# Kernel optimization log

Measured on AMD Instinct MI355X. Metric: run time of the kernel, lower is better.

## Reference

```python
import jax, jax.numpy as jnp
import numpy as np
from jax.ops import segment_sum, segment_max

H, D, HID, L, B = 4, 32, 128, 2, 64  # heads, head_dim, hidden, layers, graphs
NB, NS, NC, NF = 100000, 20000, 10000, 2000


def setup_inputs() -> dict:
    key = jax.random.key(0)
    ks = iter(jax.random.split(key, 64))
    nrm = lambda shape, s=1.0: jax.random.normal(next(ks), shape, jnp.float32) * s
    ridx = lambda n, hi: jax.random.randint(next(ks), (n,), 0, hi, jnp.int32)
    srt = lambda n, hi: jnp.sort(jax.random.randint(next(ks), (n,), 0, hi, jnp.int32))
    return {
        'x_block': nrm((NB, 8)), 'x_spmt': nrm((NS, 10)),
        'x_crane': nrm((NC, 7)), 'x_facility': nrm((NF, 3)),
        'Wp_b': nrm((8, HID), 0.2), 'bp_b': jnp.zeros((HID,), jnp.float32),
        'Wp_s': nrm((10, HID), 0.2), 'bp_s': jnp.zeros((HID,), jnp.float32),
        'Wp_c': nrm((7, HID), 0.2), 'bp_c': jnp.zeros((HID,), jnp.float32),
        'Wp_f': nrm((3, HID), 0.2), 'bp_f': jnp.zeros((HID,), jnp.float32),
        'gat_W': nrm((L, 8, HID, HID), 0.05),
        'gat_as': nrm((L, 8, H, D), 0.1), 'gat_ad': nrm((L, 8, H, D), 0.1),
        'gat_b': jnp.zeros((L, 8, HID), jnp.float32),
        'ln_s': jnp.ones((L, HID), jnp.float32), 'ln_b': jnp.zeros((L, HID), jnp.float32),
        'e_nt_s': ridx(800000, NB), 'e_nt_d': ridx(800000, NS),
        'e_ct_s': ridx(800000, NS), 'e_ct_d': ridx(800000, NB),
        'e_nl_s': ridx(400000, NB), 'e_nl_d': ridx(400000, NC),
        'e_cl_s': ridx(400000, NC), 'e_cl_d': ridx(400000, NB),
        'e_ba_s': ridx(100000, NB), 'e_ba_d': ridx(100000, NF),
        'e_pr_s': ridx(800000, NB), 'e_pr_d': ridx(800000, NB),
        'e_sa_s': ridx(20000, NS), 'e_sa_d': ridx(20000, NF),
        'e_ca_s': ridx(10000, NC), 'e_ca_d': ridx(10000, NF),
        'b_block': srt(NB, B), 'b_spmt': srt(NS, B),
        'b_crane': srt(NC, B), 'b_facility': srt(NF, B),
    }


def layer_norm(x, s, b):
    mu = x.mean(-1, keepdims=True)
    v = ((x - mu) ** 2).mean(-1, keepdims=True)
    return (x - mu) / jnp.sqrt(v + 1e-5) * s + b


def gat(h_src, h_dst, src, dst, W, a_s, a_d, bias):
    # PyG GATConv (shared lin for src/dst, add_self_loops=False, eval mode)
    n_dst = h_dst.shape[0]
    hs = (h_src @ W).reshape(-1, H, D)                 # [Ns,H,D]
    hd = (h_dst @ W).reshape(-1, H, D)                 # [Nd,H,D]
    al_s = (hs * a_s).sum(-1)                          # [Ns,H]
    al_d = (hd * a_d).sum(-1)                          # [Nd,H]
    e = jax.nn.leaky_relu(al_s[src] + al_d[dst], 0.2)  # [E,H]
    m = segment_max(e, dst, num_segments=n_dst)
    m = jnp.where(jnp.isfinite(m), m, 0.0)             # empty segments
    ex = jnp.exp(e - m[dst])
    den = segment_sum(ex, dst, num_segments=n_dst)
    coef = ex / (den[dst] + 1e-16)                     # scatter-softmax
    msg = hs[src] * coef[..., None]                    # [E,H,D]
    out = segment_sum(msg, dst, num_segments=n_dst)
    return out.reshape(n_dst, H * D) + bias


def pool(x, b):
    s = segment_sum(x, b, num_segments=B)
    c = segment_sum(jnp.ones((x.shape[0],), x.dtype), b, num_segments=B)
    return s / jnp.clip(c, 1.0)[:, None]


def reference(x_block, x_spmt, x_crane, x_facility,
              Wp_b, bp_b, Wp_s, bp_s, Wp_c, bp_c, Wp_f, bp_f,
              gat_W, gat_as, gat_ad, gat_b, ln_s, ln_b,
              e_nt_s, e_nt_d, e_ct_s, e_ct_d, e_nl_s, e_nl_d, e_cl_s, e_cl_d,
              e_ba_s, e_ba_d, e_pr_s, e_pr_d, e_sa_s, e_sa_d, e_ca_s, e_ca_d,
              b_block, b_spmt, b_crane, b_facility):
    xb = x_block @ Wp_b + bp_b
    xs = x_spmt @ Wp_s + bp_s
    xc = x_crane @ Wp_c + bp_c
    xf = x_facility @ Wp_f + bp_f
    rels = [(0, 'b', 's', e_nt_s, e_nt_d), (1, 's', 'b', e_ct_s, e_ct_d),
            (2, 'b', 'c', e_nl_s, e_nl_d), (3, 'c', 'b', e_cl_s, e_cl_d),
            (4, 'b', 'f', e_ba_s, e_ba_d), (5, 'b', 'b', e_pr_s, e_pr_d),
            (6, 's', 'f', e_sa_s, e_sa_d), (7, 'c', 'f', e_ca_s, e_ca_d)]
    for l in range(L):
        x = {'b': xb, 's': xs, 'c': xc, 'f': xf}
        acc = {k: [] for k in x}
        for r, st, dt, src, dst in rels:
            acc[dt].append(gat(x[st], x[dt], src, dst,
                               gat_W[l, r], gat_as[l, r], gat_ad[l, r], gat_b[l, r]))
        new = {k: sum(v) / len(v) for k, v in acc.items()}  # HeteroConv mean
        xb = layer_norm(jax.nn.relu(new['b']) + xb, ln_s[l], ln_b[l])
        xs = layer_norm(jax.nn.relu(new['s']) + xs, ln_s[l], ln_b[l])
        xc = layer_norm(jax.nn.relu(new['c']) + xc, ln_s[l], ln_b[l])
        xf = layer_norm(jax.nn.relu(new['f']) + xf, ln_s[l], ln_b[l])
    return jnp.concatenate([pool(xb, b_block), pool(xs, b_spmt),
                            pool(xc, b_crane), pool(xf, b_facility)], axis=-1)
```

## Files before the change

kernel.cpp:

```cpp
#include <hip/hip_runtime.h>
#include <hip/hip_bf16.h>
#include <cstdint>

#define HID 128
#define NHEAD 4
#define NGRAPH 64
#define PCHUNK 32
#define NBIN 64
#define MAXBINW 2048

typedef __attribute__((ext_vector_type(8))) short bf16x8;
typedef __attribute__((ext_vector_type(4))) short bf16x4s;
typedef __attribute__((ext_vector_type(4))) float f32x4;

__device__ __forceinline__ float bf2f(short u) {
    union { float f; unsigned int i; } c;
    c.i = ((unsigned int)(unsigned short)u) << 16;
    return c.f;
}
__device__ __forceinline__ float lrelu(float a) { return (a > 0.f) ? a : 0.2f * a; }

struct PrePack {
    const int* edst[8]; int E[8]; int h_off[9]; int bsh[8];
    int* binCnt;
    const float* px[4]; const float* pW[4]; const float* pb[4]; float* po[4];
    int pN[4]; int pK[4]; int p_off[5];
    const float* gat_W; __hip_bfloat16* Wsw;
    const float* gat_as; const float* gat_ad; float* vecall;
};

__global__ __launch_bounds__(256) void k_pre(PrePack A) {
    int b = blockIdx.x;
    int tid = threadIdx.x;
    if (b < A.h_off[8]) {
        __shared__ int h64[NBIN];
        if (tid < NBIN) h64[tid] = 0;
        __syncthreads();
#pragma unroll
        for (int r = 0; r < 8; ++r) {
            if (b >= A.h_off[r] && b < A.h_off[r + 1]) {
                int e = (b - A.h_off[r]) * 256 + tid;
                if (e < A.E[r]) atomicAdd(&h64[A.edst[r][e] >> A.bsh[r]], 1);
                __syncthreads();
                if (tid < NBIN && h64[tid] > 0) atomicAdd(&A.binCnt[r * NBIN + tid], h64[tid]);
            }
        }
        return;
    }
    b -= A.h_off[8];
    if (b < A.p_off[4]) {
#pragma unroll
        for (int t = 0; t < 4; ++t) {
            if (b >= A.p_off[t] && b < A.p_off[t + 1]) {
                int idx = (b - A.p_off[t]) * 256 + tid;
                if (idx < A.pN[t] * HID) {
                    int row = idx >> 7, c = idx & 127;
                    int K = A.pK[t];
                    float acc = A.pb[t][c];
                    for (int k = 0; k < K; ++k) acc += A.px[t][row * K + k] * A.pW[t][k * HID + c];
                    A.po[t][idx] = acc;
                }
            }
        }
        return;
    }
    b -= A.p_off[4];
    if (b < 1024) {
        int idx = b * 256 + tid;
        int l = idx >> 17;
        int rem = idx & 131071;
        int k = rem >> 10;
        int gc = rem & 1023;
        int rel, n, gobase, Ncols;
        if (gc < 512) {
            int i = gc >> 7;
            rel = (i == 0) ? 0 : (i == 1) ? 2 : (i == 2) ? 4 : 5;
            n = gc; gobase = 0; Ncols = 512;
        } else if (gc < 768) {
            int c2 = gc - 512;
            rel = (c2 >> 7) ? 6 : 1;
            n = c2; gobase = 65536; Ncols = 256;
        } else {
            int c2 = gc - 768;
            rel = (c2 >> 7) ? 7 : 3;
            n = c2; gobase = 98304; Ncols = 256;
        }
        int nl = n & 127;
        float v = A.gat_W[(((size_t)l * 8 + rel) * 128 + k) * 128 + nl];
        size_t dst = (size_t)l * 131072 + gobase + ((size_t)(k >> 3) * Ncols + n) * 8 + (k & 7);
        A.Wsw[dst] = __float2bfloat16(v);
        return;
    }
    b -= 1024;
    {
        int idx = b * 256 + tid;
        if (idx < 16384) {
            int h = idx & 3, k = (idx >> 2) & 127, p = (idx >> 9) & 15, l = idx >> 13;
            int r = p >> 1, side = p & 1;
            const float* W = A.gat_W + (((size_t)l * 8 + r) * 128 + k) * 128;
            const float* a = (side ? A.gat_ad : A.gat_as) + ((size_t)l * 8 + r) * 128;
            float s = 0.f;
#pragma unroll
            for (int j = 0; j < 32; ++j) s += W[h * 32 + j] * a[h * 32 + j];
            A.vecall[((size_t)l * 16 + p) * 512 + k * 4 + h] = s;
        }
    }
}

struct BinPack {
    const int* esrc[8]; const int* edst[8];
    uint2* staging[8];
    int* adj[8]; int* deg[8]; int* offs[8];
    int* binCnt; int* binBase; int* binCur;
    int E[8]; int Nd[8]; int binshift[8];
};

__global__ void k_binscan2(BinPack B) {
    int r = threadIdx.x;
    if (r >= 8) return;
    int run = 0;
    for (int b = 0; b < NBIN; ++b) {
        int c = B.binCnt[r * NBIN + b];
        B.binBase[r * NBIN + b] = run;
        B.binCur[r * NBIN + b] = run;
        run += c;
    }
}

__global__ __launch_bounds__(256) void k_binp1(BinPack B) {
    int r = blockIdx.y;
    int E = B.E[r];
    int sh = B.binshift[r];
    __shared__ int h[NBIN], base[NBIN], rk[NBIN];
    int tid = threadIdx.x;
    for (int e0 = blockIdx.x * 256; e0 < E; e0 += gridDim.x * 256) {
        if (tid < NBIN) { h[tid] = 0; rk[tid] = 0; }
        __syncthreads();
        int e = e0 + tid;
        int valid = e < E;
        int src = 0, dst = 0, bin = 0;
        if (valid) {
            src = B.esrc[r][e];
            dst = B.edst[r][e];
            bin = dst >> sh;
            atomicAdd(&h[bin], 1);
        }
        __syncthreads();
        if (tid < NBIN && h[tid] > 0) base[tid] = atomicAdd(&B.binCur[r * NBIN + tid], h[tid]);
        __syncthreads();
        if (valid) {
            int pos = base[bin] + atomicAdd(&rk[bin], 1);
            B.staging[r][pos] = make_uint2((unsigned)src, (unsigned)dst);
        }
        __syncthreads();
    }
}

__global__ __launch_bounds__(1024) void k_binhist(BinPack B) {
    int r = blockIdx.y, bin = blockIdx.x;
    int sh = B.binshift[r];
    int width = 1 << sh;
    int d0 = bin << sh;
    int Nd = B.Nd[r];
    int ndst = Nd - d0;
    if (ndst > width) ndst = width;
    if (ndst <= 0) return;
    __shared__ int h[MAXBINW];
    int tid = threadIdx.x;
    for (int i = tid; i < width; i += 1024) h[i] = 0;
    __syncthreads();
    int cnt = B.binCnt[r * NBIN + bin];
    const uint2* st = B.staging[r] + B.binBase[r * NBIN + bin];
    for (int i = tid; i < cnt; i += 1024) atomicAdd(&h[(int)st[i].y - d0], 1);
    __syncthreads();
    for (int i = tid; i < ndst; i += 1024) B.deg[r][d0 + i] = h[i];
}

__global__ __launch_bounds__(1024) void k_binp2(BinPack B) {
    int r = blockIdx.y, bin = blockIdx.x;
    int sh = B.binshift[r];
    int width = 1 << sh;
    int d0 = bin << sh;
    int Nd = B.Nd[r];
    int ndst = Nd - d0;
    if (ndst > width) ndst = width;
    if (ndst <= 0) return;
    __shared__ int curs[MAXBINW];
    int tid = threadIdx.x;
    for (int i = tid; i < ndst; i += 1024) curs[i] = B.offs[r][d0 + i];
    __syncthreads();
    int cnt = B.binCnt[r * NBIN + bin];
    const uint2* st = B.staging[r] + B.binBase[r * NBIN + bin];
    int* adj = B.adj[r];
    for (int i = tid; i < cnt; i += 1024) {
        uint2 ed = st[i];
        int slot = atomicAdd(&curs[(int)ed.y - d0], 1);
        adj[slot] = (int)ed.x;
    }
}

struct ScanPack {
    int* deg[8];
    int* offs[8];
    int Nd[8];
};

__global__ void k_scan_part_all(ScanPack P, int* __restrict__ part_all) {
    int r = blockIdx.y;
    int N = P.Nd[r];
    if (blockIdx.x * 256 >= N) return;
    __shared__ int sh[256];
    int t = threadIdx.x, i = blockIdx.x * 256 + t;
    sh[t] = (i < N) ? P.deg[r][i] : 0;
    __syncthreads();
    for (int o = 128; o; o >>= 1) {
        if (t < o) sh[t] += sh[t + o];
        __syncthreads();
    }
    if (t == 0) part_all[r * 512 + blockIdx.x] = sh[0];
}
__global__ void k_scan_top_all(int* __restrict__ part_all, ScanPack P) {
    int r = blockIdx.x;
    int n = (P.Nd[r] + 255) / 256;
    __shared__ int sh[512];
    int t = threadIdx.x;
    int v = (t < n) ? part_all[r * 512 + t] : 0;
    sh[t] = v;
    __syncthreads();
    for (int o = 1; o < 512; o <<= 1) {
        int tmp = (t >= o) ? sh[t - o] : 0;
        __syncthreads();
        sh[t] += tmp;
        __syncthreads();
    }
    if (t < n) part_all[r * 512 + t] = sh[t] - v;
}
__global__ void k_scan_down_all(ScanPack P, const int* __restrict__ part_all) {
    int r = blockIdx.y;
    int N = P.Nd[r];
    if (blockIdx.x * 256 >= N) return;
    __shared__ int sh[256];
    int t = threadIdx.x, i = blockIdx.x * 256 + t;
    int v = (i < N) ? P.deg[r][i] : 0;
    sh[t] = v;
    __syncthreads();
    for (int o = 1; o < 256; o <<= 1) {
        int tmp = (t >= o) ? sh[t - o] : 0;
        __syncthreads();
        sh[t] += tmp;
        __syncthreads();
    }
    if (i < N) P.offs[r][i] = sh[t] - v + part_all[r * 512 + blockIdx.x];
}

__device__ __forceinline__ void gemm_body(char* smemraw, const float* __restrict__ A,
                                          const __hip_bfloat16* __restrict__ Bsw,
                                          __hip_bfloat16* __restrict__ out,
                                          int M, int Ncols, int bx, int by) {
    __hip_bfloat16 (*Alds)[136] = (__hip_bfloat16 (*)[136])smemraw;
    int m0 = bx * 64, n0 = by * 128;
    int t = threadIdx.x;
    for (int i = t; i < 2048; i += 256) {
        int row = i >> 5, ch = i & 31;
        float4 v = make_float4(0.f, 0.f, 0.f, 0.f);
        if (m0 + row < M) v = *(const float4*)(A + (size_t)(m0 + row) * 128 + ch * 4);
        __hip_bfloat16* dp = &Alds[row][ch * 4];
        dp[0] = __float2bfloat16(v.x);
        dp[1] = __float2bfloat16(v.y);
        dp[2] = __float2bfloat16(v.z);
        dp[3] = __float2bfloat16(v.w);
    }
    __syncthreads();
    int w = t >> 6, l = t & 63;
    int lane16 = l & 15, q = l >> 4;
    f32x4 acc[8];
#pragma unroll
    for (int nn = 0; nn < 8; ++nn) acc[nn] = (f32x4){0.f, 0.f, 0.f, 0.f};
    const __hip_bfloat16* arow = &Alds[w * 16 + lane16][q * 8];
#pragma unroll
    for (int kk = 0; kk < 4; ++kk) {
        bf16x8 a = *(const bf16x8*)(arow + kk * 32);
#pragma unroll
        for (int nn = 0; nn < 8; ++nn) {
            size_t boff = ((size_t)(kk * 4 + q) * Ncols + (n0 + nn * 16 + lane16)) * 8;
            bf16x8 b = *(const bf16x8*)(Bsw + boff);
            acc[nn] = __builtin_amdgcn_mfma_f32_16x16x32_bf16(a, b, acc[nn], 0, 0, 0);
        }
    }
    int orow = m0 + w * 16 + q * 4;
#pragma unroll
    for (int nn = 0; nn < 8; ++nn) {
        int col = n0 + nn * 16 + lane16;
#pragma unroll
        for (int r = 0; r < 4; ++r) {
            int row = orow + r;
            if (row < M) out[(size_t)row * Ncols + col] = __float2bfloat16(acc[nn][r]);
        }
    }
}

__device__ __forceinline__ void logits_body(char* smemraw,
                                            const float* const vec[7], float* const outp[7],
                                            const float* __restrict__ x, int N, int nv, int bloc) {
    float (*vs)[128][4] = (float (*)[128][4])smemraw;
    int t = threadIdx.x;
    for (int i = t; i < nv * 512; i += 256) {
        int v = i >> 9, j = i & 511;
        vs[v][j >> 2][j & 3] = vec[v][j];
    }
    __syncthreads();
    int nl = t >> 2, h = t & 3;
    int node = bloc * 64 + nl;
    if (node >= N) return;
    const float* xr = x + (size_t)node * 128;
    float acc[7];
#pragma unroll
    for (int v = 0; v < 7; ++v) acc[v] = 0.f;
#pragma unroll 4
    for (int k = 0; k < 128; ++k) {
        float xv = xr[k];
#pragma unroll
        for (int v = 0; v < 7; ++v)
            if (v < nv) acc[v] += xv * vs[v][k][h];
    }
#pragma unroll
    for (int v = 0; v < 7; ++v)
        if (v < nv) outp[v][node * 4 + h] = acc[v];
}

struct MidPack {
    const float* gA[3]; const __hip_bfloat16* gB[3]; __hip_bfloat16* gO[3];
    int gM[3]; int gNc[3]; int gMB[3]; int g_off[4];
    const float* lvec[4][7]; float* lout[4][7]; const float* lx[4];
    int lN[4]; int lnv[4]; int l_off[5];
};

__global__ __launch_bounds__(256) void k_mid(MidPack M) {
    __shared__ __align__(16) char smem[17408];
    int b = blockIdx.x;
    if (b < M.g_off[3]) {
#pragma unroll
        for (int g = 0; g < 3; ++g) {
            if (b >= M.g_off[g] && b < M.g_off[g + 1]) {
                int local = b - M.g_off[g];
                int bx = local % M.gMB[g];
                int by = local / M.gMB[g];
                gemm_body(smem, M.gA[g], M.gB[g], M.gO[g], M.gM[g], M.gNc[g], bx, by);
            }
        }
        return;
    }
    b -= M.g_off[3];
#pragma unroll
    for (int t = 0; t < 4; ++t) {
        if (b >= M.l_off[t] && b < M.l_off[t + 1]) {
            logits_body(smem, M.lvec[t], M.lout[t], M.lx[t], M.lN[t], M.lnv[t], b - M.l_off[t]);
        }
    }
}

struct RelArg {
    const __hip_bfloat16* hs;
    int hstride;
    int hoff;
    const float* als;
    const float* ald;
    const int* adj;
    const int* off;
    const int* deg;
    const float* bias;
};

__device__ __forceinline__ void dst_body(const RelArg& r0, const RelArg& r1, const RelArg& r2,
                                         int nrel, float inv_nrel, float* __restrict__ x,
                                         const float* __restrict__ ln_s,
                                         const float* __restrict__ ln_b, int N, int bloc) {
    int wv = threadIdx.x >> 6, lane = threadIdx.x & 63;
    int half = lane >> 5, sl = lane & 31;
    int d = bloc * 8 + wv * 2 + half;
    if (d >= N) return;
    int c0 = sl * 4;
    int h = sl >> 3;
    float4 xv = *(const float4*)&x[(size_t)d * HID + c0];
    float rel0 = 0.f, rel1 = 0.f, rel2 = 0.f, rel3 = 0.f;
    for (int rr = 0; rr < nrel; ++rr) {
        const RelArg& R = (rr == 0) ? r0 : (rr == 1) ? r1 : r2;
        int base = R.off[d];
        int dg = R.deg[d];
        float aldh = R.ald[d * NHEAD + h];
        const __hip_bfloat16* hp = R.hs + R.hoff + c0;
        const int hstr = R.hstride;
        const int* ap = R.adj + base;
        const float* als = R.als;
        float a0 = 0.f, a1 = 0.f, a2 = 0.f, a3 = 0.f, den = 0.f;
        int k = 0;
        for (; k + 4 <= dg; k += 4) {
            int s0 = ap[k], s1 = ap[k + 1], s2 = ap[k + 2], s3 = ap[k + 3];
            float w0 = __expf(lrelu(als[s0 * NHEAD + h] + aldh));
            float w1 = __expf(lrelu(als[s1 * NHEAD + h] + aldh));
            float w2 = __expf(lrelu(als[s2 * NHEAD + h] + aldh));
            float w3 = __expf(lrelu(als[s3 * NHEAD + h] + aldh));
            bf16x4s v0 = *(const bf16x4s*)(hp + (size_t)s0 * hstr);
            bf16x4s v1 = *(const bf16x4s*)(hp + (size_t)s1 * hstr);
            bf16x4s v2 = *(const bf16x4s*)(hp + (size_t)s2 * hstr);
            bf16x4s v3 = *(const bf16x4s*)(hp + (size_t)s3 * hstr);
            a0 += w0 * bf2f(v0[0]) + w1 * bf2f(v1[0]) + w2 * bf2f(v2[0]) + w3 * bf2f(v3[0]);
            a1 += w0 * bf2f(v0[1]) + w1 * bf2f(v1[1]) + w2 * bf2f(v2[1]) + w3 * bf2f(v3[1]);
            a2 += w0 * bf2f(v0[2]) + w1 * bf2f(v1[2]) + w2 * bf2f(v2[2]) + w3 * bf2f(v3[2]);
            a3 += w0 * bf2f(v0[3]) + w1 * bf2f(v1[3]) + w2 * bf2f(v2[3]) + w3 * bf2f(v3[3]);
            den += w0 + w1 + w2 + w3;
        }
        for (; k < dg; ++k) {
            int s = ap[k];
            float w = __expf(lrelu(als[s * NHEAD + h] + aldh));
            bf16x4s v = *(const bf16x4s*)(hp + (size_t)s * hstr);
            a0 += w * bf2f(v[0]);
            a1 += w * bf2f(v[1]);
            a2 += w * bf2f(v[2]);
            a3 += w * bf2f(v[3]);
            den += w;
        }
        float inv = 1.f / (den + 1e-16f);
        rel0 += a0 * inv + R.bias[c0];
        rel1 += a1 * inv + R.bias[c0 + 1];
        rel2 += a2 * inv + R.bias[c0 + 2];
        rel3 += a3 * inv + R.bias[c0 + 3];
    }
    float v0 = rel0 * inv_nrel, v1 = rel1 * inv_nrel;
    float v2 = rel2 * inv_nrel, v3 = rel3 * inv_nrel;
    v0 = (v0 > 0.f) ? v0 : 0.f;
    v1 = (v1 > 0.f) ? v1 : 0.f;
    v2 = (v2 > 0.f) ? v2 : 0.f;
    v3 = (v3 > 0.f) ? v3 : 0.f;
    v0 += xv.x; v1 += xv.y; v2 += xv.z; v3 += xv.w;
    float s = v0 + v1 + v2 + v3;
    float ss = v0 * v0 + v1 * v1 + v2 * v2 + v3 * v3;
#pragma unroll
    for (int o = 16; o; o >>= 1) {
        s += __shfl_xor(s, o);
        ss += __shfl_xor(ss, o);
    }
    float mu = s * (1.f / HID);
    float var = ss * (1.f / HID) - mu * mu;
    float rstd = rsqrtf(var + 1e-5f);
    float o0 = (v0 - mu) * rstd * ln_s[c0] + ln_b[c0];
    float o1 = (v1 - mu) * rstd * ln_s[c0 + 1] + ln_b[c0 + 1];
    float o2 = (v2 - mu) * rstd * ln_s[c0 + 2] + ln_b[c0 + 2];
    float o3 = (v3 - mu) * rstd * ln_s[c0 + 3] + ln_b[c0 + 3];
    *(float4*)&x[(size_t)d * HID + c0] = make_float4(o0, o1, o2, o3);
}

struct TypeArg {
    RelArg r0, r1, r2;
    float* x;
    int N;
    int nrel;
    float inv_nrel;
};

__global__ __launch_bounds__(256) void k_dst_all(TypeArg t0, TypeArg t1, TypeArg t2, TypeArg t3,
                                                 int off1, int off2, int off3,
                                                 const float* __restrict__ ln_s,
                                                 const float* __restrict__ ln_b) {
    int b = blockIdx.x;
    if (b < off1) {
        dst_body(t0.r0, t0.r1, t0.r2, t0.nrel, t0.inv_nrel, t0.x, ln_s, ln_b, t0.N, b);
    } else if (b < off2) {
        dst_body(t1.r0, t1.r1, t1.r2, t1.nrel, t1.inv_nrel, t1.x, ln_s, ln_b, t1.N, b - off1);
    } else if (b < off3) {
        dst_body(t2.r0, t2.r1, t2.r2, t2.nrel, t2.inv_nrel, t2.x, ln_s, ln_b, t2.N, b - off2);
    } else {
        dst_body(t3.r0, t3.r1, t3.r2, t3.nrel, t3.inv_nrel, t3.x, ln_s, ln_b, t3.N, b - off3);
    }
}

__global__ void k_pool_all(const float* __restrict__ x0, const float* __restrict__ x1,
                           const float* __restrict__ x2, const float* __restrict__ x3,
                           const int* __restrict__ b0, const int* __restrict__ b1,
                           const int* __restrict__ b2, const int* __restrict__ b3,
                           int N0, int N1, int N2, int N3, float* __restrict__ out) {
    int ty = blockIdx.y;
    const float* x;
    const int* b;
    int N, toff;
    if (ty == 0)      { x = x0; b = b0; N = N0; toff = 0; }
    else if (ty == 1) { x = x1; b = b1; N = N1; toff = 128; }
    else if (ty == 2) { x = x2; b = b2; N = N2; toff = 256; }
    else              { x = x3; b = b3; N = N3; toff = 384; }
    int r0 = blockIdx.x * PCHUNK;
    if (r0 >= N) return;
    int rend = min(r0 + PCHUNK, N);
    int c = threadIdx.x;
    int cur = b[r0];
    float acc = 0.f;
    for (int i = r0; i < rend; ++i) {
        int g = b[i];
        if (g != cur) {
            atomicAdd(&out[cur * 512 + toff + c], acc);
            acc = 0.f;
            cur = g;
        }
        acc += x[(size_t)i * HID + c];
    }
    atomicAdd(&out[cur * 512 + toff + c], acc);
}
__global__ void k_cnt(const int* __restrict__ b0, const int* __restrict__ b1,
                      const int* __restrict__ b2, const int* __restrict__ b3,
                      int N0, int N1, int N2, int N3, float* __restrict__ cnt) {
    int i = blockIdx.x * blockDim.x + threadIdx.x;
    if (i >= 256) return;
    int t = i >> 6, g = i & 63;
    const int* b = (t == 0) ? b0 : (t == 1) ? b1 : (t == 2) ? b2 : b3;
    int N = (t == 0) ? N0 : (t == 1) ? N1 : (t == 2) ? N2 : N3;
    int lo = 0, hi = N;
    while (lo < hi) { int m = (lo + hi) >> 1; if (b[m] < g) lo = m + 1; else hi = m; }
    int s = lo;
    hi = N;
    while (lo < hi) { int m = (lo + hi) >> 1; if (b[m] < g + 1) lo = m + 1; else hi = m; }
    cnt[i] = (float)(lo - s);
}
__global__ void k_div(float* __restrict__ out, const float* __restrict__ cnt) {
    int idx = blockIdx.x * blockDim.x + threadIdx.x;
    if (idx >= NGRAPH * 512) return;
    int g = idx >> 9, c = idx & 511, t = c >> 7;
    out[idx] = out[idx] / fmaxf(cnt[t * NGRAPH + g], 1.0f);
}

extern "C" void kernel_launch(void* const* d_in, const int* in_sizes, int n_in,
                              void* d_out, int out_size, void* d_ws, size_t ws_size,
                              hipStream_t stream) {
    const float* x_in[4] = {(const float*)d_in[0], (const float*)d_in[1],
                            (const float*)d_in[2], (const float*)d_in[3]};
    const float* Wp[4] = {(const float*)d_in[4], (const float*)d_in[6],
                          (const float*)d_in[8], (const float*)d_in[10]};
    const float* bp[4] = {(const float*)d_in[5], (const float*)d_in[7],
                          (const float*)d_in[9], (const float*)d_in[11]};
    const float* gat_W  = (const float*)d_in[12];
    const float* gat_as = (const float*)d_in[13];
    const float* gat_ad = (const float*)d_in[14];
    const float* gat_b  = (const float*)d_in[15];
    const float* ln_s   = (const float*)d_in[16];
    const float* ln_b   = (const float*)d_in[17];
    const int* esrc[8] = {(const int*)d_in[18], (const int*)d_in[20], (const int*)d_in[22],
                          (const int*)d_in[24], (const int*)d_in[26], (const int*)d_in[28],
                          (const int*)d_in[30], (const int*)d_in[32]};
    const int* edst[8] = {(const int*)d_in[19], (const int*)d_in[21], (const int*)d_in[23],
                          (const int*)d_in[25], (const int*)d_in[27], (const int*)d_in[29],
                          (const int*)d_in[31], (const int*)d_in[33]};
    const int* bidx[4] = {(const int*)d_in[34], (const int*)d_in[35],
                          (const int*)d_in[36], (const int*)d_in[37]};
    int E[8];
    {
        const int eidx[8] = {18, 20, 22, 24, 26, 28, 30, 32};
        for (int r = 0; r < 8; ++r) E[r] = in_sizes[eidx[r]];
    }
    const int Kin[4] = {8, 10, 7, 3};
    int N[4];
    for (int t = 0; t < 4; ++t) N[t] = in_sizes[t] / Kin[t];
    const int rel_st[8] = {0, 1, 0, 2, 0, 0, 1, 2};
    const int rel_dt[8] = {1, 0, 2, 0, 3, 0, 3, 3};
    const int rel_hoff[8] = {0, 0, 128, 0, 256, 384, 128, 128};
    const int grp_stride[4] = {512, 256, 256, 0};
    (void)ws_size; (void)n_in;

    char* wbase = (char*)d_ws;
    size_t cur = 0;
    auto alloc = [&](size_t bytes) -> void* {
        void* p = wbase + cur;
        cur += (bytes + 15) & ~(size_t)15;
        return p;
    };
    float* x[4];
    for (int t = 0; t < 4; ++t) x[t] = (float*)alloc((size_t)N[t] * HID * 4);
    __hip_bfloat16* hs_g[3];
    hs_g[0] = (__hip_bfloat16*)alloc((size_t)N[0] * 512 * 2);
    hs_g[1] = (__hip_bfloat16*)alloc((size_t)N[1] * 256 * 2);
    hs_g[2] = (__hip_bfloat16*)alloc((size_t)N[2] * 256 * 2);
    __hip_bfloat16* Wsw = (__hip_bfloat16*)alloc((size_t)2 * 131072 * 2);
    float* vecall = (float*)alloc((size_t)2 * 16 * 512 * 4);
    float *als_[8], *ald_[8];
    int *deg[8], *offs[8], *adj[8];
    uint2* staging[8];
    for (int r = 0; r < 8; ++r) {
        int Ns = N[rel_st[r]], Nd = N[rel_dt[r]];
        als_[r] = (float*)alloc((size_t)Ns * NHEAD * 4);
        ald_[r] = (float*)alloc((size_t)Nd * NHEAD * 4);
        deg[r]  = (int*)alloc((size_t)Nd * 4);
        offs[r] = (int*)alloc((size_t)Nd * 4);
        adj[r]  = (int*)alloc((size_t)E[r] * 4);
        staging[r] = (uint2*)alloc((size_t)E[r] * 8);
    }
    int* part_all = (int*)alloc(8 * 512 * 4);
    int* binCnt   = (int*)alloc(8 * NBIN * 4);
    int* binBase  = (int*)alloc(8 * NBIN * 4);
    int* binCur   = (int*)alloc(8 * NBIN * 4);
    float* cntf   = (float*)alloc(256 * 4);

    BinPack BP;
    int NdMax = 0;
    for (int r = 0; r < 8; ++r) {
        BP.esrc[r] = esrc[r]; BP.edst[r] = edst[r];
        BP.staging[r] = staging[r];
        BP.adj[r] = adj[r]; BP.deg[r] = deg[r]; BP.offs[r] = offs[r];
        BP.E[r] = E[r]; BP.Nd[r] = N[rel_dt[r]];
        int sh = 5;
        while (((BP.Nd[r] - 1) >> sh) > (NBIN - 1)) ++sh;
        BP.binshift[r] = sh;
        if (BP.Nd[r] > NdMax) NdMax = BP.Nd[r];
    }
    BP.binCnt = binCnt; BP.binBase = binBase; BP.binCur = binCur;
    ScanPack SP;
    for (int r = 0; r < 8; ++r) { SP.deg[r] = deg[r]; SP.offs[r] = offs[r]; SP.Nd[r] = BP.Nd[r]; }

    hipMemsetAsync(binCnt, 0, 8 * NBIN * 4, stream);
    PrePack PA;
    {
        for (int r = 0; r < 8; ++r) { PA.edst[r] = edst[r]; PA.E[r] = E[r]; PA.bsh[r] = BP.binshift[r]; }
        PA.binCnt = binCnt;
        PA.h_off[0] = 0;
        for (int r = 0; r < 8; ++r) PA.h_off[r + 1] = PA.h_off[r] + (E[r] + 255) / 256;
        for (int t = 0; t < 4; ++t) {
            PA.px[t] = x_in[t]; PA.pW[t] = Wp[t]; PA.pb[t] = bp[t]; PA.po[t] = x[t];
            PA.pN[t] = N[t]; PA.pK[t] = Kin[t];
        }
        PA.p_off[0] = 0;
        for (int t = 0; t < 4; ++t) PA.p_off[t + 1] = PA.p_off[t] + (N[t] * HID + 255) / 256;
        PA.gat_W = gat_W; PA.Wsw = Wsw;
        PA.gat_as = gat_as; PA.gat_ad = gat_ad; PA.vecall = vecall;
        int total = PA.h_off[8] + PA.p_off[4] + 1024 + 64;
        k_pre<<<total, 256, 0, stream>>>(PA);
    }

    {
        k_binscan2<<<1, 64, 0, stream>>>(BP);
        dim3 g1(512, 8);
        k_binp1<<<g1, 256, 0, stream>>>(BP);
        dim3 gb(NBIN, 8);
        k_binhist<<<gb, 1024, 0, stream>>>(BP);
        dim3 gn((NdMax + 255) / 256, 8);
        k_scan_part_all<<<gn, 256, 0, stream>>>(SP, part_all);
        k_scan_top_all<<<8, 512, 0, stream>>>(part_all, SP);
        k_scan_down_all<<<gn, 256, 0, stream>>>(SP, part_all);
        k_binp2<<<gb, 1024, 0, stream>>>(BP);
    }

    hipMemsetAsync(d_out, 0, (size_t)out_size * 4, stream);
    k_cnt<<<1, 256, 0, stream>>>(bidx[0], bidx[1], bidx[2], bidx[3],
                                 N[0], N[1], N[2], N[3], cntf);

    const size_t g_woff[3] = {0, 65536, 98304};
    const int g_ncols[3] = {512, 256, 256};
    int nb[4];
    for (int t = 0; t < 4; ++t) nb[t] = (N[t] + 7) / 8;
    int doff1 = nb[0], doff2 = nb[0] + nb[1], doff3 = nb[0] + nb[1] + nb[2];
    int dtot = doff3 + nb[3];

    for (int l = 0; l < 2; ++l) {
        MidPack M;
        M.g_off[0] = 0;
        for (int g = 0; g < 3; ++g) {
            M.gA[g] = x[g];
            M.gB[g] = Wsw + (size_t)l * 131072 + g_woff[g];
            M.gO[g] = hs_g[g];
            M.gM[g] = N[g];
            M.gNc[g] = g_ncols[g];
            M.gMB[g] = (N[g] + 63) / 64;
            M.g_off[g + 1] = M.g_off[g] + M.gMB[g] * (g_ncols[g] / 128);
        }
        const float* vl = vecall + (size_t)l * 16 * 512;
        auto vvec = [&](int r, int side) { return vl + (size_t)(r * 2 + side) * 512; };
        for (int t = 0; t < 4; ++t)
            for (int v = 0; v < 7; ++v) { M.lvec[t][v] = vl; M.lout[t][v] = als_[0]; }
        M.lvec[0][0] = vvec(0, 0); M.lout[0][0] = als_[0];
        M.lvec[0][1] = vvec(2, 0); M.lout[0][1] = als_[2];
        M.lvec[0][2] = vvec(4, 0); M.lout[0][2] = als_[4];
        M.lvec[0][3] = vvec(5, 0); M.lout[0][3] = als_[5];
        M.lvec[0][4] = vvec(1, 1); M.lout[0][4] = ald_[1];
        M.lvec[0][5] = vvec(3, 1); M.lout[0][5] = ald_[3];
        M.lvec[0][6] = vvec(5, 1); M.lout[0][6] = ald_[5];
        M.lvec[1][0] = vvec(1, 0); M.lout[1][0] = als_[1];
        M.lvec[1][1] = vvec(6, 0); M.lout[1][1] = als_[6];
        M.lvec[1][2] = vvec(0, 1); M.lout[1][2] = ald_[0];
        M.lvec[2][0] = vvec(3, 0); M.lout[2][0] = als_[3];
        M.lvec[2][1] = vvec(7, 0); M.lout[2][1] = als_[7];
        M.lvec[2][2] = vvec(2, 1); M.lout[2][2] = ald_[2];
        M.lvec[3][0] = vvec(4, 1); M.lout[3][0] = ald_[4];
        M.lvec[3][1] = vvec(6, 1); M.lout[3][1] = ald_[6];
        M.lvec[3][2] = vvec(7, 1); M.lout[3][2] = ald_[7];
        const int lnv[4] = {7, 3, 3, 3};
        M.l_off[0] = 0;
        for (int t = 0; t < 4; ++t) {
            M.lx[t] = x[t]; M.lN[t] = N[t]; M.lnv[t] = lnv[t];
            M.l_off[t + 1] = M.l_off[t] + (N[t] + 63) / 64;
        }
        int total = M.g_off[3] + M.l_off[4];
        k_mid<<<total, 256, 0, stream>>>(M);

        auto mk = [&](int r) {
            RelArg a;
            int st = rel_st[r];
            a.hs = hs_g[st]; a.hstride = grp_stride[st]; a.hoff = rel_hoff[r];
            a.als = als_[r]; a.ald = ald_[r];
            a.adj = adj[r]; a.off = offs[r]; a.deg = deg[r];
            a.bias = gat_b + (size_t)(l * 8 + r) * HID;
            return a;
        };
        TypeArg T[4];
        const int trels[4][3] = {{1, 3, 5}, {0, 0, 0}, {2, 2, 2}, {4, 6, 7}};
        const int tnrel[4] = {3, 1, 1, 3};
        const float tinv[4] = {1.f / 3.f, 1.f, 1.f, 1.f / 3.f};
        for (int t = 0; t < 4; ++t) {
            T[t].r0 = mk(trels[t][0]);
            T[t].r1 = mk(trels[t][1]);
            T[t].r2 = mk(trels[t][2]);
            T[t].x = x[t];
            T[t].N = N[t];
            T[t].nrel = tnrel[t];
            T[t].inv_nrel = tinv[t];
        }
        k_dst_all<<<dtot, 256, 0, stream>>>(T[0], T[1], T[2], T[3], doff1, doff2, doff3,
                                            ln_s + l * HID, ln_b + l * HID);
    }

    {
        int pmax = 0;
        for (int t = 0; t < 4; ++t) {
            int p = (N[t] + PCHUNK - 1) / PCHUNK;
            if (p > pmax) pmax = p;
        }
        dim3 gp(pmax, 4);
        k_pool_all<<<gp, 128, 0, stream>>>(x[0], x[1], x[2], x[3],
                                           bidx[0], bidx[1], bidx[2], bidx[3],
                                           N[0], N[1], N[2], N[3], (float*)d_out);
    }
    k_div<<<(NGRAPH * 512 + 255) / 256, 256, 0, stream>>>((float*)d_out, cntf);
}
```

Baseline: 1.179 ms.

## Fuse CSR offset scan into bin histogram and loop GEMM column tiles per block

```diff
diff --git a/kernel.cpp b/kernel.cpp
--- a/kernel.cpp
+++ b/kernel.cpp
@@ -166,14 +166,28 @@
     if (ndst > width) ndst = width;
     if (ndst <= 0) return;
     __shared__ int h[MAXBINW];
+    __shared__ int s2[1024];
     int tid = threadIdx.x;
-    for (int i = tid; i < width; i += 1024) h[i] = 0;
+    for (int i = tid; i < MAXBINW; i += 1024) h[i] = 0;
     __syncthreads();
     int cnt = B.binCnt[r * NBIN + bin];
     const uint2* st = B.staging[r] + B.binBase[r * NBIN + bin];
     for (int i = tid; i < cnt; i += 1024) atomicAdd(&h[(int)st[i].y - d0], 1);
     __syncthreads();
     for (int i = tid; i < ndst; i += 1024) B.deg[r][d0 + i] = h[i];
+    int pair = h[2 * tid] + h[2 * tid + 1];
+    s2[tid] = pair;
+    __syncthreads();
+    for (int o = 1; o < 1024; o <<= 1) {
+        int v = (tid >= o) ? s2[tid - o] : 0;
+        __syncthreads();
+        s2[tid] += v;
+        __syncthreads();
+    }
+    int ebase = B.binBase[r * NBIN + bin];
+    int excl = s2[tid] - pair;
+    if (2 * tid < ndst)     B.offs[r][d0 + 2 * tid]     = ebase + excl;
+    if (2 * tid + 1 < ndst) B.offs[r][d0 + 2 * tid + 1] = ebase + excl + h[2 * tid];
 }
 
 __global__ __launch_bounds__(1024) void k_binp2(BinPack B) {
@@ -199,66 +213,12 @@
     }
 }
 
-struct ScanPack {
-    int* deg[8];
-    int* offs[8];
-    int Nd[8];
-};
-
-__global__ void k_scan_part_all(ScanPack P, int* __restrict__ part_all) {
-    int r = blockIdx.y;
-    int N = P.Nd[r];
-    if (blockIdx.x * 256 >= N) return;
-    __shared__ int sh[256];
-    int t = threadIdx.x, i = blockIdx.x * 256 + t;
-    sh[t] = (i < N) ? P.deg[r][i] : 0;
-    __syncthreads();
-    for (int o = 128; o; o >>= 1) {
-        if (t < o) sh[t] += sh[t + o];
-        __syncthreads();
-    }
-    if (t == 0) part_all[r * 512 + blockIdx.x] = sh[0];
-}
-__global__ void k_scan_top_all(int* __restrict__ part_all, ScanPack P) {
-    int r = blockIdx.x;
-    int n = (P.Nd[r] + 255) / 256;
-    __shared__ int sh[512];
-    int t = threadIdx.x;
-    int v = (t < n) ? part_all[r * 512 + t] : 0;
-    sh[t] = v;
-    __syncthreads();
-    for (int o = 1; o < 512; o <<= 1) {
-        int tmp = (t >= o) ? sh[t - o] : 0;
-        __syncthreads();
-        sh[t] += tmp;
-        __syncthreads();
-    }
-    if (t < n) part_all[r * 512 + t] = sh[t] - v;
-}
-__global__ void k_scan_down_all(ScanPack P, const int* __restrict__ part_all) {
-    int r = blockIdx.y;
-    int N = P.Nd[r];
-    if (blockIdx.x * 256 >= N) return;
-    __shared__ int sh[256];
-    int t = threadIdx.x, i = blockIdx.x * 256 + t;
-    int v = (i < N) ? P.deg[r][i] : 0;
-    sh[t] = v;
-    __syncthreads();
-    for (int o = 1; o < 256; o <<= 1) {
-        int tmp = (t >= o) ? sh[t - o] : 0;
-        __syncthreads();
-        sh[t] += tmp;
-        __syncthreads();
-    }
-    if (i < N) P.offs[r][i] = sh[t] - v + part_all[r * 512 + blockIdx.x];
-}
-
 __device__ __forceinline__ void gemm_body(char* smemraw, const float* __restrict__ A,
                                           const __hip_bfloat16* __restrict__ Bsw,
                                           __hip_bfloat16* __restrict__ out,
-                                          int M, int Ncols, int bx, int by) {
+                                          int M, int Ncols, int nby, int bx) {
     __hip_bfloat16 (*Alds)[136] = (__hip_bfloat16 (*)[136])smemraw;
-    int m0 = bx * 64, n0 = by * 128;
+    int m0 = bx * 64;
     int t = threadIdx.x;
     for (int i = t; i < 2048; i += 256) {
         int row = i >> 5, ch = i & 31;
@@ -273,28 +233,33 @@
     __syncthreads();
     int w = t >> 6, l = t & 63;
     int lane16 = l & 15, q = l >> 4;
-    f32x4 acc[8];
-#pragma unroll
-    for (int nn = 0; nn < 8; ++nn) acc[nn] = (f32x4){0.f, 0.f, 0.f, 0.f};
     const __hip_bfloat16* arow = &Alds[w * 16 + lane16][q * 8];
-#pragma unroll
-    for (int kk = 0; kk < 4; ++kk) {
-        bf16x8 a = *(const bf16x8*)(arow + kk * 32);
+    bf16x8 areg[4];
+#pragma unroll
+    for (int kk = 0; kk < 4; ++kk) areg[kk] = *(const bf16x8*)(arow + kk * 32);
+    int orow = m0 + w * 16 + q * 4;
+    for (int by = 0; by < nby; ++by) {
+        int n0 = by * 128;
+        f32x4 acc[8];
+#pragma unroll
+        for (int nn = 0; nn < 8; ++nn) acc[nn] = (f32x4){0.f, 0.f, 0.f, 0.f};
+#pragma unroll
+        for (int kk = 0; kk < 4; ++kk) {
+#pragma unroll
+            for (int nn = 0; nn < 8; ++nn) {
+                size_t boff = ((size_t)(kk * 4 + q) * Ncols + (n0 + nn * 16 + lane16)) * 8;
+                bf16x8 b = *(const bf16x8*)(Bsw + boff);
+                acc[nn] = __builtin_amdgcn_mfma_f32_16x16x32_bf16(areg[kk], b, acc[nn], 0, 0, 0);
+            }
+        }
 #pragma unroll
         for (int nn = 0; nn < 8; ++nn) {
-            size_t boff = ((size_t)(kk * 4 + q) * Ncols + (n0 + nn * 16 + lane16)) * 8;
-            bf16x8 b = *(const bf16x8*)(Bsw + boff);
-            acc[nn] = __builtin_amdgcn_mfma_f32_16x16x32_bf16(a, b, acc[nn], 0, 0, 0);
-        }
-    }
-    int orow = m0 + w * 16 + q * 4;
-#pragma unroll
-    for (int nn = 0; nn < 8; ++nn) {
-        int col = n0 + nn * 16 + lane16;
-#pragma unroll
-        for (int r = 0; r < 4; ++r) {
-            int row = orow + r;
-            if (row < M) out[(size_t)row * Ncols + col] = __float2bfloat16(acc[nn][r]);
+            int col = n0 + nn * 16 + lane16;
+#pragma unroll
+            for (int r = 0; r < 4; ++r) {
+                int row = orow + r;
+                if (row < M) out[(size_t)row * Ncols + col] = __float2bfloat16(acc[nn][r]);
+            }
         }
     }
 }
@@ -330,7 +295,7 @@
 
 struct MidPack {
     const float* gA[3]; const __hip_bfloat16* gB[3]; __hip_bfloat16* gO[3];
-    int gM[3]; int gNc[3]; int gMB[3]; int g_off[4];
+    int gM[3]; int gNc[3]; int gNB[3]; int g_off[4];
     const float* lvec[4][7]; float* lout[4][7]; const float* lx[4];
     int lN[4]; int lnv[4]; int l_off[5];
 };
@@ -342,10 +307,8 @@
 #pragma unroll
         for (int g = 0; g < 3; ++g) {
             if (b >= M.g_off[g] && b < M.g_off[g + 1]) {
-                int local = b - M.g_off[g];
-                int bx = local % M.gMB[g];
-                int by = local / M.gMB[g];
-                gemm_body(smem, M.gA[g], M.gB[g], M.gO[g], M.gM[g], M.gNc[g], bx, by);
+                gemm_body(smem, M.gA[g], M.gB[g], M.gO[g], M.gM[g], M.gNc[g], M.gNB[g],
+                          b - M.g_off[g]);
             }
         }
         return;
@@ -590,14 +553,12 @@
         adj[r]  = (int*)alloc((size_t)E[r] * 4);
         staging[r] = (uint2*)alloc((size_t)E[r] * 8);
     }
-    int* part_all = (int*)alloc(8 * 512 * 4);
     int* binCnt   = (int*)alloc(8 * NBIN * 4);
     int* binBase  = (int*)alloc(8 * NBIN * 4);
     int* binCur   = (int*)alloc(8 * NBIN * 4);
     float* cntf   = (float*)alloc(256 * 4);
 
     BinPack BP;
-    int NdMax = 0;
     for (int r = 0; r < 8; ++r) {
         BP.esrc[r] = esrc[r]; BP.edst[r] = edst[r];
         BP.staging[r] = staging[r];
@@ -606,11 +567,8 @@
         int sh = 5;
         while (((BP.Nd[r] - 1) >> sh) > (NBIN - 1)) ++sh;
         BP.binshift[r] = sh;
-        if (BP.Nd[r] > NdMax) NdMax = BP.Nd[r];
     }
     BP.binCnt = binCnt; BP.binBase = binBase; BP.binCur = binCur;
-    ScanPack SP;
-    for (int r = 0; r < 8; ++r) { SP.deg[r] = deg[r]; SP.offs[r] = offs[r]; SP.Nd[r] = BP.Nd[r]; }
 
     hipMemsetAsync(binCnt, 0, 8 * NBIN * 4, stream);
     PrePack PA;
@@ -637,10 +595,6 @@
         k_binp1<<<g1, 256, 0, stream>>>(BP);
         dim3 gb(NBIN, 8);
         k_binhist<<<gb, 1024, 0, stream>>>(BP);
-        dim3 gn((NdMax + 255) / 256, 8);
-        k_scan_part_all<<<gn, 256, 0, stream>>>(SP, part_all);
-        k_scan_top_all<<<8, 512, 0, stream>>>(part_all, SP);
-        k_scan_down_all<<<gn, 256, 0, stream>>>(SP, part_all);
         k_binp2<<<gb, 1024, 0, stream>>>(BP);
     }
 
@@ -664,8 +618,8 @@
             M.gO[g] = hs_g[g];
             M.gM[g] = N[g];
             M.gNc[g] = g_ncols[g];
-            M.gMB[g] = (N[g] + 63) / 64;
-            M.g_off[g + 1] = M.g_off[g] + M.gMB[g] * (g_ncols[g] / 128);
+            M.gNB[g] = g_ncols[g] / 128;
+            M.g_off[g + 1] = M.g_off[g] + (N[g] + 63) / 64;
         }
         const float* vl = vecall + (size_t)l * 16 * 512;
         auto vvec = [&](int r, int side) { return vl + (size_t)(r * 2 + side) * 512; };
```

Measured after the change: 1.112 ms. 1.06x faster.
